# Performance work log

Measured on AMD Instinct MI355X. Metric: run time of the kernel, lower is better.

The kernel has to match this reference:

```python
import jax, jax.numpy as jnp
import numpy as np

N = 100_000      # atoms
E = 1_600_000    # edges (avg degree 16)
B = 50           # graphs in batch
H = 128          # hidden dim
R = 50           # num radial features (emb(0.0, 6.0, 50))
MAXZ = 100
CUTOFF = 6.0
L = 3            # interaction layers (ext[1..6])


def setup_inputs() -> dict:
    key = jax.random.key(0)
    ks = jax.random.split(key, 16)
    z = jax.random.randint(ks[0], (N,), 0, MAXZ)
    pos = jax.random.normal(ks[1], (N, 3), dtype=jnp.float32) * 3.0
    cell = jnp.eye(3, dtype=jnp.float32)[None] * 10.0 + 0.1 * jax.random.normal(ks[2], (B, 3, 3), dtype=jnp.float32)
    edge_index = jax.random.randint(ks[3], (2, E), 0, N)
    cell_offsets = jax.random.randint(ks[4], (E, 3), -1, 2)  # {-1,0,1}
    edge_batch = jax.random.randint(ks[5], (E,), 0, B)
    # learned parameters
    atom_emb = jax.random.normal(ks[6], (MAXZ, H), dtype=jnp.float32) * 0.1
    dist_table = jax.random.normal(ks[7], (R, R), dtype=jnp.float32) * 0.1  # dist_emb embedding table
    s_e = 1.0 / np.sqrt(2 * H + R)
    s_h = 1.0 / np.sqrt(H)
    We = jax.random.normal(ks[8], (L, 2 * H + R, H), dtype=jnp.float32) * s_e
    be = jnp.zeros((L, H), dtype=jnp.float32)
    Wv = jax.random.normal(ks[9], (L, H, H), dtype=jnp.float32) * s_h
    bv = jnp.zeros((L, H), dtype=jnp.float32)
    Wh = jax.random.normal(ks[10], (H, H), dtype=jnp.float32) * s_h
    bh = jnp.zeros((H,), dtype=jnp.float32)
    return dict(z=z, pos=pos, cell=cell, edge_index=edge_index,
                cell_offsets=cell_offsets, edge_batch=edge_batch,
                atom_emb=atom_emb, dist_table=dist_table,
                We=We, be=be, Wv=Wv, bv=bv, Wh=Wh, bh=bh)


def reference(z, pos, cell, edge_index, cell_offsets, edge_batch,
              atom_emb, dist_table, We, be, Wv, bv, Wh, bh):
    row, col = edge_index[0], edge_index[1]
    # get_pbc_distances: offsets = cell_offsets @ per-edge cell
    off = jnp.einsum('ek,ekl->el', cell_offsets.astype(jnp.float32), cell[edge_batch])  # [E,3]
    vec = pos[row] - pos[col] + off
    dist = jnp.sqrt(jnp.sum(vec * vec, axis=-1))  # [E]
    # dist_emb(dist.to(long)): integer-cast distance indexes the embedding table
    demb = dist_table[jnp.clip(dist.astype(jnp.int32), 0, R - 1)]  # [E,R]
    env = 0.5 * (jnp.cos(jnp.pi * jnp.clip(dist, 0.0, CUTOFF) / CUTOFF) + 1.0)  # cosine cutoff [E]
    v = atom_emb[z]  # ext[0]: atom embedding [N,H]
    for i in range(L):
        # ext[2i+1]: edge layer — gather endpoints, concat with radial features
        m = jnp.concatenate([v[row], v[col], demb], axis=-1)  # [E, 2H+R]
        e = jax.nn.silu(m @ We[i] + be[i]) * env[:, None]     # [E, H]
        # ext[2i+2]: node layer — scatter-sum messages to destination nodes
        agg = jax.ops.segment_sum(e, col, num_segments=N)     # [N, H]
        v = v + jax.nn.silu(agg @ Wv[i] + bv[i])
    v = v @ Wh + bh  # head
    return (v, pos, dist)
```

## Files before the change

### kernel.cpp

```cpp
#include <hip/hip_runtime.h>
#include <hip/hip_bf16.h>

#define HID 128
#define RR 50
#define NLAY 3
#define CBSH 9
#define CBSZ 512
#define CPAD (CBSZ * 3)
#define ACHUNK 8192

typedef __attribute__((ext_vector_type(8))) short short8;
typedef __attribute__((ext_vector_type(4))) float f32x4;
typedef __attribute__((ext_vector_type(2))) float f32x2;

static __device__ __forceinline__ unsigned short f2bf(float x) {
    unsigned int b = __builtin_bit_cast(unsigned int, x);
    b = b + 0x7FFFu + ((b >> 16) & 1u);
    return (unsigned short)(b >> 16);
}
static __device__ __forceinline__ float bf2f(unsigned int u) {
    return __builtin_bit_cast(float, u << 16);
}
static __device__ __forceinline__ f32x2 bfpair(unsigned u) {
    f32x2 r;
    r.x = __builtin_bit_cast(float, u << 16);
    r.y = __builtin_bit_cast(float, u & 0xffff0000u);
    return r;
}
static __device__ __forceinline__ float silu_f(float x) {
    float e = __expf(-x);
    return x * __builtin_amdgcn_rcpf(1.0f + e);
}

__global__ __launch_bounds__(256) void k_geom(
    const int* __restrict__ ei, const int* __restrict__ co,
    const int* __restrict__ eb, const float* __restrict__ cell,
    const float* __restrict__ pos, float* __restrict__ dist_out,
    int2* __restrict__ rec, int* __restrict__ ccol,
    float* __restrict__ out_pos, int N3, int E)
{
    int e = blockIdx.x * 256 + threadIdx.x;
    if (e < N3) out_pos[e] = pos[e];
    if (e >= E) return;
    int r = ei[e], c = ei[E + e], b = eb[e];
    float c0 = (float)co[3*e], c1 = (float)co[3*e+1], c2 = (float)co[3*e+2];
    const float* cb = cell + b * 9;
    float v0 = pos[3*r+0] - pos[3*c+0] + c0*cb[0] + c1*cb[3] + c2*cb[6];
    float v1 = pos[3*r+1] - pos[3*c+1] + c0*cb[1] + c1*cb[4] + c2*cb[7];
    float v2 = pos[3*r+2] - pos[3*c+2] + c0*cb[2] + c1*cb[5] + c2*cb[8];
    float d = sqrtf(v0*v0 + v1*v1 + v2*v2);
    dist_out[e] = d;
    bool keep = d < 6.0f;
    ccol[e] = keep ? c : -1;
    if (keep) {
        int di = (int)d;
        di = di < 0 ? 0 : (di > RR - 1 ? RR - 1 : di);
        float envv = 0.5f * (cosf(d * (3.14159265358979323846f / 6.0f)) + 1.0f);
        rec[e] = make_int2((r << 8) | di, __builtin_bit_cast(int, envv));
    }
}

__global__ __launch_bounds__(256) void k_cntA(
    const int* __restrict__ col, int* __restrict__ gb, int E, int nCB)
{
    __shared__ int lc[1024];
    int tid = threadIdx.x;
    for (int i = tid; i < nCB; i += 256) lc[i] = 0;
    __syncthreads();
    int base = blockIdx.x * ACHUNK;
    int end = base + ACHUNK; if (end > E) end = E;
    for (int e = base + tid; e < end; e += 256) {
        int c = col[e];
        if (c >= 0) atomicAdd(&lc[((unsigned)c) >> CBSH], 1);
    }
    __syncthreads();
    for (int i = tid; i < nCB; i += 256)
        if (lc[i]) atomicAdd(&gb[i], lc[i]);
}

__global__ __launch_bounds__(256) void k_projz(
    const int* __restrict__ z, const unsigned short* __restrict__ P12t,
    unsigned short* __restrict__ P1, int N)
{
    int gid = blockIdx.x * 256 + threadIdx.x;
    if (gid >= N * 16) return;
    int n = gid >> 4, c4 = gid & 15;
    int zz = z[n];
    uint4 t1 = *(const uint4*)(P12t + (size_t)zz * 256 + c4 * 8);
    *(uint4*)(P1 + (size_t)n * HID + c4 * 8) = t1;
}

__global__ __launch_bounds__(256) void k_wprep(
    const float* __restrict__ We, const float* __restrict__ Wv,
    const float* __restrict__ Wh, const float* __restrict__ dt,
    const float* __restrict__ be, const float* __restrict__ emb,
    unsigned short* __restrict__ WvP, unsigned short* __restrict__ WcP,
    unsigned short* __restrict__ WhP, unsigned short* __restrict__ TbP,
    unsigned short* __restrict__ P12t)
{
    int blk = blockIdx.x;
    if (blk < 640) {
        int t = blk * 256 + threadIdx.x;
        int j = t & 7, l = (t >> 3) & 63, s = (t >> 9) & 3;
        int ln = l & 15, g = l >> 4;
        int k = s * 32 + g * 4 + (j & 3) + ((j >> 2) << 4);
        if (t < 3 * 16384) {
            int i = t >> 14; int nt = (t >> 11) & 7;
            WvP[t] = f2bf(Wv[(size_t)i * 16384 + k * HID + nt * 16 + ln]);
        } else if (t < 3 * 16384 + 3 * 32768) {
            int u = t - 3 * 16384; int i = u >> 15; int nt = (u >> 11) & 15;
            int col = nt * 16 + ln;
            float val = (col < HID) ? We[(size_t)i * 306 * HID + k * HID + col]
                                    : We[(size_t)i * 306 * HID + (HID + k) * HID + (col - HID)];
            WcP[u] = f2bf(val);
        } else {
            int u = t - 3 * 16384 - 3 * 32768; int nt = (u >> 11) & 7;
            WhP[u] = f2bf(Wh[k * HID + nt * 16 + ln]);
        }
    } else if (blk < 640 + NLAY * RR) {
        if (threadIdx.x >= HID) return;
        int row = blk - 640;
        int i = row / RR, r = row % RR;
        int c = threadIdx.x;
        float s = be[i * HID + c];
        const float* w = We + (size_t)i * 306 * HID + 256 * HID + c;
        const float* dr = dt + r * RR;
        for (int k = 0; k < RR; ++k) s += dr[k] * w[k * HID];
        TbP[(i * RR + r) * HID + c] = f2bf(s);
    } else {
        int zz = blk - 640 - NLAY * RR;
        int c = threadIdx.x;
        int cm = c & 127, half = c >> 7;
        const float* er = emb + (size_t)zz * HID;
        const float* w = We + (size_t)(half * 128) * HID + cm;
        float s = 0.f;
        #pragma unroll 8
        for (int k = 0; k < 128; ++k) s += er[k] * w[k * HID];
        P12t[(size_t)zz * 256 + c] = f2bf(s);
    }
}

__global__ __launch_bounds__(256) void k_scanA(
    const int* __restrict__ gb, int* __restrict__ gbase,
    int* __restrict__ gcur, int nCB)
{
    __shared__ int ps[256];
    __shared__ int carry;
    int t = threadIdx.x;
    if (t == 0) carry = 0;
    __syncthreads();
    for (int base = 0; base < nCB; base += 256) {
        int v = (base + t < nCB) ? gb[base + t] : 0;
        ps[t] = v; __syncthreads();
        for (int d = 1; d < 256; d <<= 1) {
            int x = (t >= d) ? ps[t - d] : 0;
            __syncthreads();
            ps[t] += x;
            __syncthreads();
        }
        int excl = carry + ps[t] - v;
        if (base + t < nCB) { gbase[base + t] = excl; gcur[base + t] = excl; }
        __syncthreads();
        if (t == 0) carry += ps[255];
        __syncthreads();
    }
    if (t == 0) gbase[nCB] = carry;
}

__global__ __launch_bounds__(256) void k_splitA(
    const int* __restrict__ col, const int2* __restrict__ rec,
    int* __restrict__ gcur, int2* __restrict__ binned,
    int* __restrict__ bcol, int E, int nCB)
{
    __shared__ int lc[1024];
    __shared__ int lres[1024];
    int tid = threadIdx.x;
    for (int i = tid; i < nCB; i += 256) lc[i] = 0;
    __syncthreads();
    int base = blockIdx.x * ACHUNK;
    int end = base + ACHUNK; if (end > E) end = E;
    for (int e = base + tid; e < end; e += 256) {
        int c = col[e];
        if (c >= 0) atomicAdd(&lc[((unsigned)c) >> CBSH], 1);
    }
    __syncthreads();
    for (int i = tid; i < nCB; i += 256) {
        lres[i] = lc[i] ? atomicAdd(&gcur[i], lc[i]) : 0;
        lc[i] = 0;
    }
    __syncthreads();
    for (int e = base + tid; e < end; e += 256) {
        int c = col[e];
        if (c < 0) continue;
        int b = ((unsigned)c) >> CBSH;
        int rank = atomicAdd(&lc[b], 1);
        int p = lres[b] + rank;
        binned[p] = rec[e];
        bcol[p] = c;
    }
}

__global__ __launch_bounds__(256) void k_sortB(
    const int2* __restrict__ binned, const int* __restrict__ bcol,
    const int* __restrict__ gbase, int2* __restrict__ meta,
    int2* __restrict__ noff, int N)
{
    __shared__ int lcnt[CBSZ], lcur[CBSZ], pscan[CBSZ];
    __shared__ int wsum[64];
    const int b = blockIdx.x;
    const int tid = threadIdx.x;
    const int s = gbase[b], e = gbase[b + 1];
    const int mbase = s + b * CPAD;
    for (int i = tid; i < CBSZ; i += 256) { lcnt[i] = 0; lcur[i] = 0; }
    __syncthreads();
    for (int t = s + tid; t < e; t += 256)
        atomicAdd(&lcnt[bcol[t] & (CBSZ - 1)], 1);
    __syncthreads();
    if (tid < 64) {
        int ssum = 0;
        #pragma unroll
        for (int k = 0; k < 8; ++k) {
            int idx = tid * 8 + k;
            int pc = (lcnt[idx] + 3) & ~3;
            pscan[idx] = ssum;
            ssum += pc;
        }
        wsum[tid] = ssum;
    }
    __syncthreads();
    if (tid == 0) {
        int c = 0;
        for (int i = 0; i < 64; ++i) { int t = wsum[i]; wsum[i] = c; c += t; }
    }
    __syncthreads();
    if (tid < 64) {
        #pragma unroll
        for (int k = 0; k < 8; ++k) pscan[tid * 8 + k] += wsum[tid];
    }
    __syncthreads();
    for (int i = tid; i < CBSZ; i += 256) {
        int node = (b << CBSH) + i;
        if (node < N) {
            noff[node] = make_int2(mbase + pscan[i], lcnt[i]);
            int pb = mbase + pscan[i] + lcnt[i];
            int pads = ((lcnt[i] + 3) & ~3) - lcnt[i];
            for (int k = 0; k < pads; ++k) meta[pb + k] = make_int2(0, 0);
        }
    }
    __syncthreads();
    for (int t = s + tid; t < e; t += 256) {
        int local = bcol[t] & (CBSZ - 1);
        int rank = atomicAdd(&lcur[local], 1);
        meta[mbase + pscan[local] + rank] = binned[t];
    }
}

#define PLD(M) (*(const unsigned*)(P1b + (unsigned)((((unsigned)(M).x) & 0xFFFFFF00u) | lane4)))
#define TLDG(M) (*(const unsigned*)(Tb_ + (((((unsigned)(M).x) & 255u) << 8) | lane4)))

#define EP(GG, TBU, MM)                                                       \
    {                                                                         \
        f32x2 xx = bfpair(GG) + (bfpair(TBU) + p2v);                          \
        f32x2 nx = xx * -1.442695041f;                                        \
        f32x2 ee;                                                             \
        ee.x = __builtin_amdgcn_exp2f(nx.x);                                  \
        ee.y = __builtin_amdgcn_exp2f(nx.y);                                  \
        f32x2 dd = ee + 1.0f;                                                 \
        f32x2 rr;                                                             \
        rr.x = __builtin_amdgcn_rcpf(dd.x);                                   \
        rr.y = __builtin_amdgcn_rcpf(dd.y);                                   \
        f32x2 sl = xx * rr;                                                   \
        float evf = __builtin_bit_cast(float, (MM).y);                        \
        av += sl * evf;                                                       \
    }

static __device__ __forceinline__ short8 ldfrag(const unsigned short* A, int r, int s, int g) {
    const char* p = (const char*)(A + r * 136) + s * 64 + g * 8;
    uint2 lo = *(const uint2*)p;
    uint2 hi = *(const uint2*)(p + 32);
    uint4 u; u.x = lo.x; u.y = lo.y; u.z = hi.x; u.w = hi.y;
    return __builtin_bit_cast(short8, u);
}

template<int NT2, bool FINAL, bool FIRST>
__global__ __launch_bounds__(512) void k_layer(
    const unsigned short* __restrict__ P1,
    const unsigned short* __restrict__ P2,
    const unsigned short* __restrict__ TbBf,
    const int2* __restrict__ meta,
    const int2* __restrict__ noff,
    const int* __restrict__ z,
    const float* __restrict__ emb,
    const unsigned short* __restrict__ P12t,
    const unsigned short* __restrict__ B1p,
    const float* __restrict__ b1,
    unsigned short* __restrict__ v,
    const unsigned short* __restrict__ B2p,
    const float* __restrict__ b2,
    unsigned short* __restrict__ P1d,
    unsigned short* __restrict__ P2d,
    float* __restrict__ outd, int N)
{
    __shared__ __align__(16) unsigned short SHB[2 * 32 * 136];
    unsigned short* SH  = SHB;
    unsigned short* SHV = SHB + 32 * 136;
    const int tid = threadIdx.x;
    const int node0 = blockIdx.x * 32;
    const int w = tid >> 6, l = tid & 63, g = (l >> 4) & 3, ln = l & 15;
    const int lane = l;
    const unsigned lane4 = 4u * (unsigned)lane;

    {
        int r = tid >> 4, c = tid & 15;
        uint4 y4 = make_uint4(0, 0, 0, 0);
        if (node0 + r < N) {
            if (FIRST) {
                int zz = z[node0 + r];
                const float4* ep = (const float4*)(emb + (size_t)zz * HID) + c * 2;
                float4 a = ep[0], b = ep[1];
                y4.x = ((unsigned)f2bf(a.y) << 16) | f2bf(a.x);
                y4.y = ((unsigned)f2bf(a.w) << 16) | f2bf(a.z);
                y4.z = ((unsigned)f2bf(b.y) << 16) | f2bf(b.x);
                y4.w = ((unsigned)f2bf(b.w) << 16) | f2bf(b.z);
            } else {
                y4 = *(const uint4*)(v + (size_t)(node0 + r) * HID + c * 8);
            }
        }
        *(uint4*)(SHV + r * 136 + c * 8) = y4;
    }

    short8 bf1[4];
    #pragma unroll
    for (int s = 0; s < 4; ++s)
        bf1[s] = *(const short8*)(B1p + ((w * 4 + s) * 64 + l) * 8);

    {
        const char* P1b = (const char*)P1;
        const char* Tb_ = (const char*)TbBf;
        const int r0 = w << 2;
        int2 ni = make_int2(0, 0);
        int zq = 0;
        {
            int pn = node0 + r0 + lane;
            if (lane < 4 && pn < N) {
                ni = noff[pn];
                if (FIRST) zq = z[pn];
            }
        }
        #pragma unroll 1
        for (int i = 0; i < 4; ++i) {
            int r = r0 + i;
            unsigned* outp = (unsigned*)(SH + r * 136 + 2 * lane);
            int n = __builtin_amdgcn_readlane(ni.y, i);
            if (n == 0) { *outp = 0u; continue; }
            int s = __builtin_amdgcn_readlane(ni.x, i);
            int node = node0 + r;
            unsigned p2u;
            if (FIRST) {
                int zz = __builtin_amdgcn_readlane(zq, i);
                p2u = *(const unsigned*)(P12t + (size_t)zz * 256 + 128 + 2 * lane);
            } else {
                p2u = *(const unsigned*)(P2 + (size_t)node * HID + 2 * lane);
            }
            n = (n + 3) & ~3;
            f32x2 p2v = bfpair(p2u);
            f32x2 av; av.x = 0.f; av.y = 0.f;
            const int2* mp = meta + s;
            int2 m0 = mp[0], m1 = mp[1], m2 = mp[2], m3 = mp[3];
            unsigned g0 = PLD(m0), g1 = PLD(m1), g2 = PLD(m2), g3 = PLD(m3);
            for (int t = 0; t < n; t += 4) {
                int2 n0 = mp[t + 4], n1 = mp[t + 5], n2 = mp[t + 6], n3 = mp[t + 7];
                unsigned h0 = PLD(n0), h1 = PLD(n1), h2 = PLD(n2), h3 = PLD(n3);
                unsigned t0 = TLDG(m0), t1 = TLDG(m1), t2 = TLDG(m2), t3 = TLDG(m3);
                EP(g0, t0, m0) EP(g1, t1, m1) EP(g2, t2, m2) EP(g3, t3, m3)
                m0 = n0; m1 = n1; m2 = n2; m3 = n3;
                g0 = h0; g1 = h1; g2 = h2; g3 = h3;
            }
            *outp = (((unsigned)f2bf(av.y)) << 16) | (unsigned)f2bf(av.x);
        }
    }

    {
        __syncthreads();
        f32x4 acc[2] = {};
        #pragma unroll
        for (int s = 0; s < 4; ++s)
            #pragma unroll
            for (int mt = 0; mt < 2; ++mt) {
                short8 af = ldfrag(SH, 16 * mt + ln, s, g);
                acc[mt] = __builtin_amdgcn_mfma_f32_16x16x32_bf16(af, bf1[s], acc[mt], 0, 0, 0);
            }
        __syncthreads();
        float bvc = b1[16 * w + ln];
        #pragma unroll
        for (int mt = 0; mt < 2; ++mt) {
            int col = 16 * w + ln;
            #pragma unroll
            for (int j = 0; j < 4; ++j) {
                int r = 16 * mt + 4 * g + j;
                float y = silu_f(acc[mt][j] + bvc);
                float vn = bf2f((unsigned)SHV[r * 136 + col]) + y;
                SH[r * 136 + col] = f2bf(vn);
            }
        }
        __syncthreads();
        if (!FINAL) {
            int r = tid >> 4, c = tid & 15;
            if (node0 + r < N)
                *(uint4*)(v + (size_t)(node0 + r) * HID + c * 8) =
                    *(const uint4*)(SH + r * 136 + c * 8);
        }
    }

    constexpr int NTW = NT2 / 8;
    short8 bf2[NTW][4];
    #pragma unroll
    for (int nt = 0; nt < NTW; ++nt)
        #pragma unroll
        for (int s = 0; s < 4; ++s)
            bf2[nt][s] = *(const short8*)(B2p + (((w * NTW + nt) * 4 + s) * 64 + l) * 8);
    f32x4 acc2[2][NTW] = {};
    #pragma unroll
    for (int s = 0; s < 4; ++s)
        #pragma unroll
        for (int mt = 0; mt < 2; ++mt) {
            short8 af = ldfrag(SH, 16 * mt + ln, s, g);
            #pragma unroll
            for (int nt = 0; nt < NTW; ++nt)
                acc2[mt][nt] = __builtin_amdgcn_mfma_f32_16x16x32_bf16(af, bf2[nt][s], acc2[mt][nt], 0, 0, 0);
        }
    __syncthreads();
    if (FINAL) {
        float* fst = (float*)SHB;
        int col = w * 16 + ln;
        float bb = b2[col];
        #pragma unroll
        for (int mt = 0; mt < 2; ++mt)
            #pragma unroll
            for (int j = 0; j < 4; ++j) {
                int r = 16 * mt + 4 * g + j;
                fst[r * 132 + col] = acc2[mt][0][j] + bb;
            }
        __syncthreads();
        #pragma unroll
        for (int i = 0; i < 2; ++i) {
            int u = tid + 512 * i, r = u >> 5, cg = u & 31;
            if (node0 + r < N)
                *(float4*)(outd + (size_t)(node0 + r) * HID + cg * 4) =
                    *(const float4*)(fst + r * 132 + cg * 4);
        }
    } else {
        #pragma unroll
        for (int nt = 0; nt < NTW; ++nt) {
            int gidx = w * NTW + nt;
            int colm = (gidx * 16 + ln) & 127;
            unsigned short* dst = (gidx < 8) ? SHV : SH;
            #pragma unroll
            for (int mt = 0; mt < 2; ++mt)
                #pragma unroll
                for (int j = 0; j < 4; ++j) {
                    int r = 16 * mt + 4 * g + j;
                    dst[r * 136 + colm] = f2bf(acc2[mt][nt][j]);
                }
        }
        __syncthreads();
        {
            int r = tid >> 4, cg = tid & 15;
            if (node0 + r < N) {
                *(uint4*)(P1d + (size_t)(node0 + r) * HID + cg * 8) =
                    *(const uint4*)(SHV + r * 136 + cg * 8);
                *(uint4*)(P2d + (size_t)(node0 + r) * HID + cg * 8) =
                    *(const uint4*)(SH + r * 136 + cg * 8);
            }
        }
    }
}

extern "C" void kernel_launch(void* const* d_in, const int* in_sizes, int n_in,
                              void* d_out, int out_size, void* d_ws, size_t ws_size,
                              hipStream_t stream)
{
    const int*   z    = (const int*)d_in[0];
    const float* pos  = (const float*)d_in[1];
    const float* cell = (const float*)d_in[2];
    const int*   ei   = (const int*)d_in[3];
    const int*   co   = (const int*)d_in[4];
    const int*   eb   = (const int*)d_in[5];
    const float* emb  = (const float*)d_in[6];
    const float* dt   = (const float*)d_in[7];
    const float* We   = (const float*)d_in[8];
    const float* be   = (const float*)d_in[9];
    const float* Wv   = (const float*)d_in[10];
    const float* bv   = (const float*)d_in[11];
    const float* Wh   = (const float*)d_in[12];
    const float* bh   = (const float*)d_in[13];

    const int N = in_sizes[0];
    const int E = in_sizes[5];
    const int MAXZ = in_sizes[6] / HID;
    const int nCB = (N + CBSZ - 1) >> CBSH;
    const size_t metaN = (size_t)E + (size_t)nCB * CPAD + 32;

    char* p = (char*)d_ws;
    unsigned short* v    = (unsigned short*)p;  p += (size_t)N * HID * 2;
    unsigned short* P1a  = (unsigned short*)p;  p += (size_t)N * HID * 2;
    unsigned short* P1b  = (unsigned short*)p;  p += (size_t)N * HID * 2;
    unsigned short* P2   = (unsigned short*)p;  p += (size_t)N * HID * 2;
    int2*  meta  = (int2*)p;                    p += metaN * 8;
    int2*  noff  = (int2*)p;                    p += (size_t)N * 8;
    int*   gb    = (int*)p;                     p += (size_t)(nCB + 1) * 4;
    int*   gbase = (int*)p;                     p += (size_t)(nCB + 1) * 4;
    int*   gcur  = (int*)p;                     p += (size_t)(nCB + 1) * 4;
    unsigned short* TbP = (unsigned short*)p;   p += (size_t)NLAY * RR * HID * 2;
    unsigned short* WvP = (unsigned short*)p;   p += (size_t)3 * 16384 * 2;
    unsigned short* WcP = (unsigned short*)p;   p += (size_t)3 * 32768 * 2;
    unsigned short* WhP = (unsigned short*)p;   p += (size_t)16384 * 2;
    unsigned short* P12t = (unsigned short*)p;  p += (size_t)MAXZ * 256 * 2;

    int2* rec    = (int2*)P1a;
    int2* binned = (int2*)((char*)P1a + (size_t)E * 8);
    int*  ccol   = (int*)P2;
    int*  bcol   = (int*)((char*)P2 + (size_t)E * 4);

    float* out_v    = (float*)d_out;
    float* out_pos  = out_v + (size_t)N * HID;
    float* out_dist = out_pos + (size_t)N * 3;

    const int nlayer = (N + 31) / 32;
    const int nblkA = (E + ACHUNK - 1) / ACHUNK;
    const int N3 = N * 3;
    int ngeom = (E + 255) / 256;
    if ((N3 + 255) / 256 > ngeom) ngeom = (N3 + 255) / 256;

    hipMemsetAsync(gb, 0, (size_t)(nCB + 1) * 4, stream);
    hipMemsetAsync(meta, 0, metaN * 8, stream);
    k_geom<<<ngeom, 256, 0, stream>>>(ei, co, eb, cell, pos, out_dist, rec, ccol,
                                      out_pos, N3, E);
    k_cntA<<<nblkA, 256, 0, stream>>>(ccol, gb, E, nCB);
    k_scanA<<<1, 256, 0, stream>>>(gb, gbase, gcur, nCB);
    k_splitA<<<nblkA, 256, 0, stream>>>(ccol, rec, gcur, binned, bcol, E, nCB);
    k_sortB<<<nCB, 256, 0, stream>>>(binned, bcol, gbase, meta, noff, N);

    k_wprep<<<640 + NLAY * RR + MAXZ, 256, 0, stream>>>(
        We, Wv, Wh, dt, be, emb, WvP, WcP, WhP, TbP, P12t);

    k_projz<<<(N * 16 + 255) / 256, 256, 0, stream>>>(z, P12t, P1a, N);

    k_layer<16, false, true><<<nlayer, 512, 0, stream>>>(
        P1a, nullptr, TbP, meta, noff, z, emb, P12t,
        WvP, bv, v, WcP + (size_t)32768, nullptr, P1b, P2, nullptr, N);
    k_layer<16, false, false><<<nlayer, 512, 0, stream>>>(
        P1b, P2, TbP + (size_t)RR * HID, meta, noff, nullptr, nullptr, nullptr,
        WvP + (size_t)16384, bv + (size_t)HID, v,
        WcP + (size_t)2 * 32768, nullptr, P1a, P2, nullptr, N);
    k_layer<8, true, false><<<nlayer, 512, 0, stream>>>(
        P1a, P2, TbP + (size_t)2 * RR * HID, meta, noff, nullptr, nullptr, nullptr,
        WvP + (size_t)2 * 16384, bv + (size_t)2 * HID, v,
        WhP, bh, nullptr, nullptr, out_v, N);
}
```

Baseline: 202.6 us.

## Recompute destination-node projection in-block instead of storing and reloading P2

```diff
diff --git a/kernel.cpp b/kernel.cpp
--- a/kernel.cpp
+++ b/kernel.cpp
@@ -282,28 +282,28 @@
     return __builtin_bit_cast(short8, u);
 }
 
-template<int NT2, bool FINAL, bool FIRST>
+template<bool FINAL, bool FIRST>
 __global__ __launch_bounds__(512) void k_layer(
     const unsigned short* __restrict__ P1,
-    const unsigned short* __restrict__ P2,
     const unsigned short* __restrict__ TbBf,
     const int2* __restrict__ meta,
     const int2* __restrict__ noff,
     const int* __restrict__ z,
     const float* __restrict__ emb,
     const unsigned short* __restrict__ P12t,
+    const unsigned short* __restrict__ Wp2,
     const unsigned short* __restrict__ B1p,
     const float* __restrict__ b1,
     unsigned short* __restrict__ v,
     const unsigned short* __restrict__ B2p,
     const float* __restrict__ b2,
     unsigned short* __restrict__ P1d,
-    unsigned short* __restrict__ P2d,
     float* __restrict__ outd, int N)
 {
-    __shared__ __align__(16) unsigned short SHB[2 * 32 * 136];
+    __shared__ __align__(16) unsigned short SHB[3 * 32 * 136];
     unsigned short* SH  = SHB;
     unsigned short* SHV = SHB + 32 * 136;
+    unsigned short* SHP = SHB + 2 * 32 * 136;
     const int tid = threadIdx.x;
     const int node0 = blockIdx.x * 32;
     const int w = tid >> 6, l = tid & 63, g = (l >> 4) & 3, ln = l & 15;
@@ -334,6 +334,32 @@
     for (int s = 0; s < 4; ++s)
         bf1[s] = *(const short8*)(B1p + ((w * 4 + s) * 64 + l) * 8);
 
+    if (!FIRST) {
+        short8 bfp2[4];
+        #pragma unroll
+        for (int s = 0; s < 4; ++s)
+            bfp2[s] = *(const short8*)(Wp2 + ((((8 + w) * 4 + s)) * 64 + l) * 8);
+        __syncthreads();
+        f32x4 accp[2] = {};
+        #pragma unroll
+        for (int s = 0; s < 4; ++s)
+            #pragma unroll
+            for (int mt = 0; mt < 2; ++mt) {
+                short8 af = ldfrag(SHV, 16 * mt + ln, s, g);
+                accp[mt] = __builtin_amdgcn_mfma_f32_16x16x32_bf16(af, bfp2[s], accp[mt], 0, 0, 0);
+            }
+        #pragma unroll
+        for (int mt = 0; mt < 2; ++mt) {
+            int col = 16 * w + ln;
+            #pragma unroll
+            for (int j = 0; j < 4; ++j) {
+                int r = 16 * mt + 4 * g + j;
+                SHP[r * 136 + col] = f2bf(accp[mt][j]);
+            }
+        }
+        __syncthreads();
+    }
+
     {
         const char* P1b = (const char*)P1;
         const char* Tb_ = (const char*)TbBf;
@@ -354,13 +380,12 @@
             int n = __builtin_amdgcn_readlane(ni.y, i);
             if (n == 0) { *outp = 0u; continue; }
             int s = __builtin_amdgcn_readlane(ni.x, i);
-            int node = node0 + r;
             unsigned p2u;
             if (FIRST) {
                 int zz = __builtin_amdgcn_readlane(zq, i);
                 p2u = *(const unsigned*)(P12t + (size_t)zz * 256 + 128 + 2 * lane);
             } else {
-                p2u = *(const unsigned*)(P2 + (size_t)node * HID + 2 * lane);
+                p2u = *(const unsigned*)(SHP + r * 136 + 2 * lane);
             }
             n = (n + 3) & ~3;
             f32x2 p2v = bfpair(p2u);
@@ -412,22 +437,17 @@
         }
     }
 
-    constexpr int NTW = NT2 / 8;
-    short8 bf2[NTW][4];
-    #pragma unroll
-    for (int nt = 0; nt < NTW; ++nt)
-        #pragma unroll
-        for (int s = 0; s < 4; ++s)
-            bf2[nt][s] = *(const short8*)(B2p + (((w * NTW + nt) * 4 + s) * 64 + l) * 8);
-    f32x4 acc2[2][NTW] = {};
+    short8 bf2[4];
     #pragma unroll
     for (int s = 0; s < 4; ++s)
+        bf2[s] = *(const short8*)(B2p + ((w * 4 + s) * 64 + l) * 8);
+    f32x4 acc2[2] = {};
+    #pragma unroll
+    for (int s = 0; s < 4; ++s)
         #pragma unroll
         for (int mt = 0; mt < 2; ++mt) {
             short8 af = ldfrag(SH, 16 * mt + ln, s, g);
-            #pragma unroll
-            for (int nt = 0; nt < NTW; ++nt)
-                acc2[mt][nt] = __builtin_amdgcn_mfma_f32_16x16x32_bf16(af, bf2[nt][s], acc2[mt][nt], 0, 0, 0);
+            acc2[mt] = __builtin_amdgcn_mfma_f32_16x16x32_bf16(af, bf2[s], acc2[mt], 0, 0, 0);
         }
     __syncthreads();
     if (FINAL) {
@@ -439,7 +459,7 @@
             #pragma unroll
             for (int j = 0; j < 4; ++j) {
                 int r = 16 * mt + 4 * g + j;
-                fst[r * 132 + col] = acc2[mt][0][j] + bb;
+                fst[r * 132 + col] = acc2[mt][j] + bb;
             }
         __syncthreads();
         #pragma unroll
@@ -450,28 +470,22 @@
                     *(const float4*)(fst + r * 132 + cg * 4);
         }
     } else {
-        #pragma unroll
-        for (int nt = 0; nt < NTW; ++nt) {
-            int gidx = w * NTW + nt;
-            int colm = (gidx * 16 + ln) & 127;
-            unsigned short* dst = (gidx < 8) ? SHV : SH;
+        {
+            int col = w * 16 + ln;
             #pragma unroll
             for (int mt = 0; mt < 2; ++mt)
                 #pragma unroll
                 for (int j = 0; j < 4; ++j) {
                     int r = 16 * mt + 4 * g + j;
-                    dst[r * 136 + colm] = f2bf(acc2[mt][nt][j]);
+                    SHV[r * 136 + col] = f2bf(acc2[mt][j]);
                 }
         }
         __syncthreads();
         {
             int r = tid >> 4, cg = tid & 15;
-            if (node0 + r < N) {
+            if (node0 + r < N)
                 *(uint4*)(P1d + (size_t)(node0 + r) * HID + cg * 8) =
                     *(const uint4*)(SHV + r * 136 + cg * 8);
-                *(uint4*)(P2d + (size_t)(node0 + r) * HID + cg * 8) =
-                    *(const uint4*)(SH + r * 136 + cg * 8);
-            }
         }
     }
 }
@@ -505,7 +519,7 @@
     unsigned short* v    = (unsigned short*)p;  p += (size_t)N * HID * 2;
     unsigned short* P1a  = (unsigned short*)p;  p += (size_t)N * HID * 2;
     unsigned short* P1b  = (unsigned short*)p;  p += (size_t)N * HID * 2;
-    unsigned short* P2   = (unsigned short*)p;  p += (size_t)N * HID * 2;
+    unsigned short* scr  = (unsigned short*)p;  p += (size_t)N * HID * 2;
     int2*  meta  = (int2*)p;                    p += metaN * 8;
     int2*  noff  = (int2*)p;                    p += (size_t)N * 8;
     int*   gb    = (int*)p;                     p += (size_t)(nCB + 1) * 4;
@@ -519,8 +533,8 @@
 
     int2* rec    = (int2*)P1a;
     int2* binned = (int2*)((char*)P1a + (size_t)E * 8);
-    int*  ccol   = (int*)P2;
-    int*  bcol   = (int*)((char*)P2 + (size_t)E * 4);
+    int*  ccol   = (int*)scr;
+    int*  bcol   = (int*)((char*)scr + (size_t)E * 4);
 
     float* out_v    = (float*)d_out;
     float* out_pos  = out_v + (size_t)N * HID;
@@ -546,15 +560,17 @@
 
     k_projz<<<(N * 16 + 255) / 256, 256, 0, stream>>>(z, P12t, P1a, N);
 
-    k_layer<16, false, true><<<nlayer, 512, 0, stream>>>(
-        P1a, nullptr, TbP, meta, noff, z, emb, P12t,
-        WvP, bv, v, WcP + (size_t)32768, nullptr, P1b, P2, nullptr, N);
-    k_layer<16, false, false><<<nlayer, 512, 0, stream>>>(
-        P1b, P2, TbP + (size_t)RR * HID, meta, noff, nullptr, nullptr, nullptr,
+    k_layer<false, true><<<nlayer, 512, 0, stream>>>(
+        P1a, TbP, meta, noff, z, emb, P12t, nullptr,
+        WvP, bv, v, WcP + (size_t)32768, nullptr, P1b, nullptr, N);
+    k_layer<false, false><<<nlayer, 512, 0, stream>>>(
+        P1b, TbP + (size_t)RR * HID, meta, noff, nullptr, nullptr, nullptr,
+        WcP + (size_t)32768,
         WvP + (size_t)16384, bv + (size_t)HID, v,
-        WcP + (size_t)2 * 32768, nullptr, P1a, P2, nullptr, N);
-    k_layer<8, true, false><<<nlayer, 512, 0, stream>>>(
-        P1a, P2, TbP + (size_t)2 * RR * HID, meta, noff, nullptr, nullptr, nullptr,
+        WcP + (size_t)2 * 32768, nullptr, P1a, nullptr, N);
+    k_layer<true, false><<<nlayer, 512, 0, stream>>>(
+        P1a, TbP + (size_t)2 * RR * HID, meta, noff, nullptr, nullptr, nullptr,
+        WcP + (size_t)2 * 32768,
         WvP + (size_t)2 * 16384, bv + (size_t)2 * HID, v,
-        WhP, bh, nullptr, nullptr, out_v, N);
-}
+        WhP, bh, nullptr, out_v, N);
+}
```

New measurement: 205.9 us. About the same (+1.6%).
